# Performance work log

Hardware: AMD Instinct MI355X
Metric: run time of the kernel (lower is better)

Reference implementation:

```python
import jax, jax.numpy as jnp
import numpy as np


def setup_inputs() -> dict:
    key = jax.random.key(0)
    k1, k2, k3, k4, k5 = jax.random.split(key, 5)
    C, S = 256, 16  # in_channels, se_channels
    x = jax.random.normal(k1, (64, C, 56, 56), dtype=jnp.float32)
    # 1x1 conv weights stored as [out, in] (kernel spatial dims are 1x1)
    w1 = jax.random.normal(k2, (S, C), dtype=jnp.float32) * (1.0 / np.sqrt(C))
    b1 = jax.random.normal(k3, (S,), dtype=jnp.float32) * 0.01
    w2 = jax.random.normal(k4, (C, S), dtype=jnp.float32) * (1.0 / np.sqrt(S))
    b2 = jax.random.normal(k5, (C,), dtype=jnp.float32) * 0.01
    return {"x": x, "w1": w1, "b1": b1, "w2": w2, "b2": b2}


def reference(x, w1, b1, w2, b2):
    # squeeze: global average pool over H, W -> [N, C]
    s = jnp.mean(x, axis=(2, 3))
    # excitation: 1x1 conv MLP with swish then sigmoid gate
    h = jnp.einsum('nc,sc->ns', s, w1) + b1          # [N, S]
    h = h * jax.nn.sigmoid(h)                        # swish
    g = jax.nn.sigmoid(jnp.einsum('ns,cs->nc', h, w2) + b2)  # [N, C]
    # broadcast multiply back over spatial dims
    return x * g[:, :, None, None]
```

## Files before the change

### kernel.cpp

```cpp
#include <hip/hip_runtime.h>
#include <math.h>

#define N_  64
#define C_  256
#define S_  16
#define HW_ 3136
#define HW4_ 784

typedef float f32x4 __attribute__((ext_vector_type(4)));

__global__ __launch_bounds__(256) void se_pool(const float* __restrict__ x,
                                               float* __restrict__ s) {
    const int row = blockIdx.x;
    const f32x4* xr = reinterpret_cast<const f32x4*>(x + (size_t)row * HW_);
    float sum = 0.f;
    for (int i = threadIdx.x; i < HW4_; i += 256) {
        f32x4 v = xr[i];
        sum += (v.x + v.y) + (v.z + v.w);
    }
    #pragma unroll
    for (int off = 32; off; off >>= 1) sum += __shfl_down(sum, off, 64);
    __shared__ float partial[4];
    const int wave = threadIdx.x >> 6;
    const int lane = threadIdx.x & 63;
    if (lane == 0) partial[wave] = sum;
    __syncthreads();
    if (threadIdx.x == 0) {
        float t = (partial[0] + partial[1]) + (partial[2] + partial[3]);
        s[row] = t * (1.0f / (float)HW_);
    }
}

__device__ __forceinline__ float sigmoidf_(float v) {
    return 1.0f / (1.0f + expf(-v));
}

__global__ __launch_bounds__(256) void se_mlp(const float* __restrict__ s,
                                              const float* __restrict__ w1,
                                              const float* __restrict__ b1,
                                              const float* __restrict__ w2,
                                              const float* __restrict__ b2,
                                              float* __restrict__ g) {
    const int n = blockIdx.x;
    const int t = threadIdx.x;
    __shared__ float s_sh[C_];
    __shared__ float h_sh[S_];
    s_sh[t] = s[n * C_ + t];
    __syncthreads();

    const int j  = t >> 4;
    const int sl = t & 15;
    float p = 0.f;
    #pragma unroll
    for (int k = sl; k < C_; k += 16) p += s_sh[k] * w1[j * C_ + k];
    #pragma unroll
    for (int m = 8; m; m >>= 1) p += __shfl_xor(p, m, 64);
    if (sl == 0) {
        float hv = p + b1[j];
        h_sh[j] = hv * sigmoidf_(hv);
    }
    __syncthreads();

    float acc = b2[t];
    #pragma unroll
    for (int k = 0; k < S_; ++k) acc += h_sh[k] * w2[t * S_ + k];
    g[n * C_ + t] = sigmoidf_(acc);
}

__global__ __launch_bounds__(256) void se_scale(const float* __restrict__ x,
                                                const float* __restrict__ g,
                                                float* __restrict__ out) {
    const int row = blockIdx.x;
    const float gv = g[row];
    const f32x4* xr = reinterpret_cast<const f32x4*>(x + (size_t)row * HW_);
    f32x4* orow = reinterpret_cast<f32x4*>(out + (size_t)row * HW_);
    for (int i = threadIdx.x; i < HW4_; i += 256) {
        f32x4 v = xr[i];
        v *= gv;
        __builtin_nontemporal_store(v, &orow[i]);
    }
}

extern "C" void kernel_launch(void* const* d_in, const int* in_sizes, int n_in,
                              void* d_out, int out_size, void* d_ws, size_t ws_size,
                              hipStream_t stream) {
    const float* x  = (const float*)d_in[0];
    const float* w1 = (const float*)d_in[1];
    const float* b1 = (const float*)d_in[2];
    const float* w2 = (const float*)d_in[3];
    const float* b2 = (const float*)d_in[4];
    float* out = (float*)d_out;

    float* s = (float*)d_ws;
    float* g = s + N_ * C_;

    se_pool<<<N_ * C_, 256, 0, stream>>>(x, s);
    se_mlp<<<N_, 256, 0, stream>>>(s, w1, b1, w2, b2, g);
    se_scale<<<N_ * C_, 256, 0, stream>>>(x, g, out);
}
```

Baseline: 99.56 us.

## Fuse pool, MLP and scale into one cooperative persistent kernel

```diff
diff --git a/kernel.cpp b/kernel.cpp
--- a/kernel.cpp
+++ b/kernel.cpp
@@ -1,83 +1,89 @@
 #include <hip/hip_runtime.h>
+#include <hip/hip_cooperative_groups.h>
 #include <math.h>
 
-#define N_  64
-#define C_  256
-#define S_  16
-#define HW_ 3136
+namespace cg = cooperative_groups;
+
+#define N_   64
+#define C_   256
+#define S_   16
+#define HW_  3136
 #define HW4_ 784
+#define ROWS_   (N_ * C_)
+#define BLOCKS_ 1024
+#define RPB_    (ROWS_ / BLOCKS_)
+#define RPW_    (RPB_ / 4)
 
 typedef float f32x4 __attribute__((ext_vector_type(4)));
-
-__global__ __launch_bounds__(256) void se_pool(const float* __restrict__ x,
-                                               float* __restrict__ s) {
-    const int row = blockIdx.x;
-    const f32x4* xr = reinterpret_cast<const f32x4*>(x + (size_t)row * HW_);
-    float sum = 0.f;
-    for (int i = threadIdx.x; i < HW4_; i += 256) {
-        f32x4 v = xr[i];
-        sum += (v.x + v.y) + (v.z + v.w);
-    }
-    #pragma unroll
-    for (int off = 32; off; off >>= 1) sum += __shfl_down(sum, off, 64);
-    __shared__ float partial[4];
-    const int wave = threadIdx.x >> 6;
-    const int lane = threadIdx.x & 63;
-    if (lane == 0) partial[wave] = sum;
-    __syncthreads();
-    if (threadIdx.x == 0) {
-        float t = (partial[0] + partial[1]) + (partial[2] + partial[3]);
-        s[row] = t * (1.0f / (float)HW_);
-    }
-}
 
 __device__ __forceinline__ float sigmoidf_(float v) {
     return 1.0f / (1.0f + expf(-v));
 }
 
-__global__ __launch_bounds__(256) void se_mlp(const float* __restrict__ s,
-                                              const float* __restrict__ w1,
-                                              const float* __restrict__ b1,
-                                              const float* __restrict__ w2,
-                                              const float* __restrict__ b2,
-                                              float* __restrict__ g) {
-    const int n = blockIdx.x;
-    const int t = threadIdx.x;
+__global__ __launch_bounds__(256, 4) void se_fused(
+    const float* __restrict__ x,
+    const float* __restrict__ w1, const float* __restrict__ b1,
+    const float* __restrict__ w2, const float* __restrict__ b2,
+    float* __restrict__ out, float* __restrict__ s, float* __restrict__ g)
+{
+    cg::grid_group grid = cg::this_grid();
+    const int t    = threadIdx.x;
+    const int wave = t >> 6;
+    const int lane = t & 63;
+    const int base = blockIdx.x * RPB_;
+
     __shared__ float s_sh[C_];
     __shared__ float h_sh[S_];
-    s_sh[t] = s[n * C_ + t];
-    __syncthreads();
 
-    const int j  = t >> 4;
-    const int sl = t & 15;
-    float p = 0.f;
     #pragma unroll
-    for (int k = sl; k < C_; k += 16) p += s_sh[k] * w1[j * C_ + k];
+    for (int rr = 0; rr < RPW_; ++rr) {
+        const int row = base + wave * RPW_ + rr;
+        const f32x4* xr = reinterpret_cast<const f32x4*>(x + (size_t)row * HW_);
+        float sum = 0.f;
+        for (int i = lane; i < HW4_; i += 64) {
+            f32x4 v = xr[i];
+            sum += (v.x + v.y) + (v.z + v.w);
+        }
+        #pragma unroll
+        for (int off = 32; off; off >>= 1) sum += __shfl_down(sum, off, 64);
+        if (lane == 0) s[row] = sum * (1.0f / (float)HW_);
+    }
+    grid.sync();
+
+    if (blockIdx.x < N_) {
+        const int n = blockIdx.x;
+        s_sh[t] = s[n * C_ + t];
+        __syncthreads();
+        const int j  = t >> 4;
+        const int sl = t & 15;
+        float p = 0.f;
+        #pragma unroll
+        for (int k = sl; k < C_; k += 16) p += s_sh[k] * w1[j * C_ + k];
+        #pragma unroll
+        for (int m = 8; m; m >>= 1) p += __shfl_xor(p, m, 64);
+        if (sl == 0) {
+            float hv = p + b1[j];
+            h_sh[j] = hv * sigmoidf_(hv);
+        }
+        __syncthreads();
+        float acc = b2[t];
+        #pragma unroll
+        for (int k = 0; k < S_; ++k) acc += h_sh[k] * w2[t * S_ + k];
+        g[n * C_ + t] = sigmoidf_(acc);
+    }
+    grid.sync();
+
     #pragma unroll
-    for (int m = 8; m; m >>= 1) p += __shfl_xor(p, m, 64);
-    if (sl == 0) {
-        float hv = p + b1[j];
-        h_sh[j] = hv * sigmoidf_(hv);
-    }
-    __syncthreads();
-
-    float acc = b2[t];
-    #pragma unroll
-    for (int k = 0; k < S_; ++k) acc += h_sh[k] * w2[t * S_ + k];
-    g[n * C_ + t] = sigmoidf_(acc);
-}
-
-__global__ __launch_bounds__(256) void se_scale(const float* __restrict__ x,
-                                                const float* __restrict__ g,
-                                                float* __restrict__ out) {
-    const int row = blockIdx.x;
-    const float gv = g[row];
-    const f32x4* xr = reinterpret_cast<const f32x4*>(x + (size_t)row * HW_);
-    f32x4* orow = reinterpret_cast<f32x4*>(out + (size_t)row * HW_);
-    for (int i = threadIdx.x; i < HW4_; i += 256) {
-        f32x4 v = xr[i];
-        v *= gv;
-        __builtin_nontemporal_store(v, &orow[i]);
+    for (int rr = 0; rr < RPW_; ++rr) {
+        const int row = base + wave * RPW_ + rr;
+        const float gv = g[row];
+        const f32x4* xr = reinterpret_cast<const f32x4*>(x + (size_t)row * HW_);
+        f32x4* orow = reinterpret_cast<f32x4*>(out + (size_t)row * HW_);
+        for (int i = lane; i < HW4_; i += 64) {
+            f32x4 v = xr[i];
+            v *= gv;
+            __builtin_nontemporal_store(v, &orow[i]);
+        }
     }
 }
 
@@ -94,7 +100,8 @@
     float* s = (float*)d_ws;
     float* g = s + N_ * C_;
 
-    se_pool<<<N_ * C_, 256, 0, stream>>>(x, s);
-    se_mlp<<<N_, 256, 0, stream>>>(s, w1, b1, w2, b2, g);
-    se_scale<<<N_ * C_, 256, 0, stream>>>(x, g, out);
+    void* args[] = { (void*)&x, (void*)&w1, (void*)&b1, (void*)&w2, (void*)&b2,
+                     (void*)&out, (void*)&s, (void*)&g };
+    hipLaunchCooperativeKernel((const void*)se_fused, dim3(BLOCKS_), dim3(256),
+                               args, 0, stream);
 }
```

After: 273.5 us. 2.75x slower.
